# Kernel optimization log

Hardware: AMD Instinct MI355X
Metric: run time of the kernel (lower is better)

Reference implementation:

```python
import jax, jax.numpy as jnp
import numpy as np
from jax import lax

RADIUS = 2  # scipy grey_opening(x, 2): flat 2x2 structuring element


def _grey_opening2d(x, r=RADIUS):
    """Channel-wise grey opening (erosion then dilation) with a flat r x r
    structuring element, matching scipy.ndimage.grey_opening(x, r) with its
    default 'reflect' boundary (edge replication suffices for pad width <= 1
    here; offsets follow scipy's origin convention for even sizes, which makes
    erosion/dilation an adjoint pair so opening(x) <= x and is idempotent).
    x: [B, C, H, W]
    """
    lo = r // 2          # pad-before for erosion (offsets -(r//2) .. r-r//2-1)
    hi = r - 1 - r // 2  # pad-after for erosion
    # erosion: windowed min
    xp = jnp.pad(x, ((0, 0), (0, 0), (lo, hi), (lo, hi)), mode='edge')
    er = lax.reduce_window(xp, jnp.array(jnp.inf, x.dtype), lax.min,
                           (1, 1, r, r), (1, 1, 1, 1), 'VALID')
    # dilation: windowed max with adjoint (mirrored) offsets
    ep = jnp.pad(er, ((0, 0), (0, 0), (hi, lo), (hi, lo)), mode='edge')
    op = lax.reduce_window(ep, jnp.array(-jnp.inf, x.dtype), lax.max,
                           (1, 1, r, r), (1, 1, 1, 1), 'VALID')
    return op


def setup_inputs() -> dict:
    key = jax.random.key(0)
    labels = jax.random.uniform(key, (16, 8, 512, 512), dtype=jnp.float32)
    return {"labels": labels}


def reference(labels):
    smooth = _grey_opening2d(labels)           # detached target in original
    diff = labels - lax.stop_gradient(smooth)
    return jnp.mean(diff * diff)               # nn.MSELoss default 'mean'
```

## Files before the change

### kernel.cpp

```cpp
#include <hip/hip_runtime.h>

#define HH 512
#define WW 512
#define STRIP 16
#define SPI (HH / STRIP)
#define NTASK (128 * SPI)
#define BLOCK 256
#define WPB 4
#define NBLK (NTASK / WPB)
#define NSLOT (STRIP + 2)
#define DEPTH 2
#define NTOTAL (16.0 * 8.0 * 512.0 * 512.0)

__global__ __launch_bounds__(BLOCK, 4) void opening_partial(
    const float* __restrict__ x, float* __restrict__ partial)
{
    const int wb    = (blockIdx.x & 7) * (NBLK / 8) + (blockIdx.x >> 3);
    const int lane  = threadIdx.x & 63;
    const int wid   = wb * WPB + (threadIdx.x >> 6);
    const int img   = wid >> 5;
    const int strip = wid & (SPI - 1);
    const int r0    = strip * STRIP;
    const bool bot  = (strip == SPI - 1);

    const float* ib = x + (size_t)img * (HH * WW);
    const int cA  = lane * 4;
    const int cB  = 256 + lane * 4;
    const int cAm = (lane == 0) ? 0 : cA - 1;
    const int cBm = cB - 1;
    const int cAp = cA + 4;
    const int cBp = (cB + 4 > WW - 1) ? (WW - 1) : (cB + 4);
    const bool rcl = (cB + 4 > WW - 1);

    float RA[NSLOT][6], RB[NSLOT][6];

#define LOADS(s, r)                                                       \
    do {                                                                  \
        const float* rowp = ib + (size_t)(r) * WW;                        \
        const float4 a4 = *(const float4*)(rowp + cA);                    \
        const float4 b4 = *(const float4*)(rowp + cB);                    \
        RA[s][0] = rowp[cAm]; RA[s][1] = a4.x; RA[s][2] = a4.y;           \
        RA[s][3] = a4.z;      RA[s][4] = a4.w; RA[s][5] = rowp[cAp];      \
        RB[s][0] = rowp[cBm]; RB[s][1] = b4.x; RB[s][2] = b4.y;           \
        RB[s][3] = b4.z;      RB[s][4] = b4.w; RB[s][5] = rowp[cBp];      \
    } while (0)

#define RCROW(s, rc)                                                      \
    do {                                                                  \
        rc[0] = fminf(RA[s][0], RA[s][1]); rc[1] = fminf(RA[s][1], RA[s][2]); \
        rc[2] = fminf(RA[s][2], RA[s][3]); rc[3] = fminf(RA[s][3], RA[s][4]); \
        rc[4] = fminf(RA[s][4], RA[s][5]);                                \
        rc[5] = fminf(RB[s][0], RB[s][1]); rc[6] = fminf(RB[s][1], RB[s][2]); \
        rc[7] = fminf(RB[s][2], RB[s][3]); rc[8] = fminf(RB[s][3], RB[s][4]); \
        rc[9] = rcl ? rc[8] : fminf(RB[s][4], RB[s][5]);                  \
    } while (0)

#define CLAMPR(r) (((r) < 0) ? 0 : (((r) > HH - 1) ? (HH - 1) : (r)))

    float rp[10], dp[8];
    float acc = 0.f;

#pragma unroll
    for (int s = 0; s < DEPTH; ++s) LOADS(s, CLAMPR(r0 - 1 + s));

#pragma unroll
    for (int s = 0; s < NSLOT - 1; ++s) {
        if (s + DEPTH < NSLOT) LOADS(s + DEPTH, CLAMPR(r0 - 1 + s + DEPTH));
        float rc[10];
        RCROW(s, rc);
        if (s == 0) {
#pragma unroll
            for (int j = 0; j < 10; ++j) rp[j] = rc[j];
        } else {
            float er[10], d[8];
#pragma unroll
            for (int j = 0; j < 10; ++j) er[j] = fminf(rp[j], rc[j]);
#pragma unroll
            for (int j = 0; j < 4; ++j) {
                d[j]     = fmaxf(er[j], er[j + 1]);
                d[4 + j] = fmaxf(er[5 + j], er[6 + j]);
            }
            if (s >= 2) {
#pragma unroll
                for (int j = 0; j < 4; ++j) {
                    const float oA = fmaxf(dp[j], d[j]);
                    const float oB = fmaxf(dp[4 + j], d[4 + j]);
                    const float fA = RA[s - 1][j + 1] - oA;
                    const float fB = RB[s - 1][j + 1] - oB;
                    acc = fmaf(fA, fA, acc);
                    acc = fmaf(fB, fB, acc);
                }
            }
#pragma unroll
            for (int j = 0; j < 10; ++j) rp[j] = rc[j];
#pragma unroll
            for (int j = 0; j < 8; ++j) dp[j] = d[j];
        }
    }

    if (!bot) {
        float rc[10];
        RCROW(NSLOT - 1, rc);
        float er[10];
#pragma unroll
        for (int j = 0; j < 10; ++j) er[j] = fminf(rp[j], rc[j]);
#pragma unroll
        for (int j = 0; j < 4; ++j) {
            const float dA = fmaxf(er[j], er[j + 1]);
            const float dB = fmaxf(er[5 + j], er[6 + j]);
            const float fA = RA[NSLOT - 2][j + 1] - fmaxf(dp[j], dA);
            const float fB = RB[NSLOT - 2][j + 1] - fmaxf(dp[4 + j], dB);
            acc = fmaf(fA, fA, acc);
            acc = fmaf(fB, fB, acc);
        }
    } else {
#pragma unroll
        for (int j = 0; j < 4; ++j) {
            const float fA = RA[NSLOT - 2][j + 1] - dp[j];
            const float fB = RB[NSLOT - 2][j + 1] - dp[4 + j];
            acc = fmaf(fA, fA, acc);
            acc = fmaf(fB, fB, acc);
        }
    }
#undef LOADS
#undef RCROW
#undef CLAMPR

    __shared__ float wsum[WPB];
#pragma unroll
    for (int off = 32; off; off >>= 1) acc += __shfl_down(acc, off);
    if (lane == 0) wsum[threadIdx.x >> 6] = acc;
    __syncthreads();
    if (threadIdx.x == 0)
        partial[blockIdx.x] = (wsum[0] + wsum[1]) + (wsum[2] + wsum[3]);
}

__global__ __launch_bounds__(256) void reduce_final(
    const float* __restrict__ partial, float* __restrict__ out)
{
    __shared__ double sm[256];
    const int t = threadIdx.x;
    double s = 0.0;
#pragma unroll
    for (int i = 0; i < NBLK / 256; ++i) s += (double)partial[t + 256 * i];
    sm[t] = s;
    __syncthreads();
    for (int h = 128; h > 0; h >>= 1) {
        if (t < h) sm[t] += sm[t + h];
        __syncthreads();
    }
    if (t == 0) out[0] = (float)(sm[0] / NTOTAL);
}

extern "C" void kernel_launch(void* const* d_in, const int* in_sizes, int n_in,
                              void* d_out, int out_size, void* d_ws, size_t ws_size,
                              hipStream_t stream)
{
    const float* x = (const float*)d_in[0];
    float* partial = (float*)d_ws;
    float* out = (float*)d_out;

    opening_partial<<<NBLK, BLOCK, 0, stream>>>(x, partial);
    reduce_final<<<1, 256, 0, stream>>>(partial, out);
}
```

Baseline: 29.06 us.

## Split each strip across two wavefronts, one per image half-width

Each wavefront now covers one 256-column half of a 16-row strip instead of the full 512 columns. This doubles the number of waves and blocks and halves the per-thread register arrays, and the launch bound is raised to 8 blocks per CU to allow higher occupancy. The cost is more redundant halo loads at column and row boundaries, and twice as many partial sums for the final reduction to read.

```diff
diff --git a/kernel.cpp b/kernel.cpp
--- a/kernel.cpp
+++ b/kernel.cpp
@@ -4,7 +4,7 @@
 #define WW 512
 #define STRIP 16
 #define SPI (HH / STRIP)
-#define NTASK (128 * SPI)
+#define NTASK (128 * SPI * 2)
 #define BLOCK 256
 #define WPB 4
 #define NBLK (NTASK / WPB)
@@ -12,52 +12,44 @@
 #define DEPTH 2
 #define NTOTAL (16.0 * 8.0 * 512.0 * 512.0)
 
-__global__ __launch_bounds__(BLOCK, 4) void opening_partial(
+__global__ __launch_bounds__(BLOCK, 8) void opening_partial(
     const float* __restrict__ x, float* __restrict__ partial)
 {
     const int wb    = (blockIdx.x & 7) * (NBLK / 8) + (blockIdx.x >> 3);
     const int lane  = threadIdx.x & 63;
     const int wid   = wb * WPB + (threadIdx.x >> 6);
-    const int img   = wid >> 5;
-    const int strip = wid & (SPI - 1);
+    const int img   = wid >> 6;
+    const int half  = wid & 1;
+    const int strip = (wid >> 1) & (SPI - 1);
     const int r0    = strip * STRIP;
     const bool bot  = (strip == SPI - 1);
 
     const float* ib = x + (size_t)img * (HH * WW);
-    const int cA  = lane * 4;
-    const int cB  = 256 + lane * 4;
-    const int cAm = (lane == 0) ? 0 : cA - 1;
-    const int cBm = cB - 1;
-    const int cAp = cA + 4;
-    const int cBp = (cB + 4 > WW - 1) ? (WW - 1) : (cB + 4);
-    const bool rcl = (cB + 4 > WW - 1);
+    const int c   = half * 256 + lane * 4;
+    const int cm  = (c == 0) ? 0 : c - 1;
+    const int cp  = (c + 4 > WW - 1) ? (WW - 1) : (c + 4);
+    const bool rcl = (c + 4 > WW - 1);
 
-    float RA[NSLOT][6], RB[NSLOT][6];
+    float R[NSLOT][6];
 
 #define LOADS(s, r)                                                       \
     do {                                                                  \
         const float* rowp = ib + (size_t)(r) * WW;                        \
-        const float4 a4 = *(const float4*)(rowp + cA);                    \
-        const float4 b4 = *(const float4*)(rowp + cB);                    \
-        RA[s][0] = rowp[cAm]; RA[s][1] = a4.x; RA[s][2] = a4.y;           \
-        RA[s][3] = a4.z;      RA[s][4] = a4.w; RA[s][5] = rowp[cAp];      \
-        RB[s][0] = rowp[cBm]; RB[s][1] = b4.x; RB[s][2] = b4.y;           \
-        RB[s][3] = b4.z;      RB[s][4] = b4.w; RB[s][5] = rowp[cBp];      \
+        const float4 a4 = *(const float4*)(rowp + c);                     \
+        R[s][0] = rowp[cm]; R[s][1] = a4.x; R[s][2] = a4.y;               \
+        R[s][3] = a4.z;     R[s][4] = a4.w; R[s][5] = rowp[cp];           \
     } while (0)
 
 #define RCROW(s, rc)                                                      \
     do {                                                                  \
-        rc[0] = fminf(RA[s][0], RA[s][1]); rc[1] = fminf(RA[s][1], RA[s][2]); \
-        rc[2] = fminf(RA[s][2], RA[s][3]); rc[3] = fminf(RA[s][3], RA[s][4]); \
-        rc[4] = fminf(RA[s][4], RA[s][5]);                                \
-        rc[5] = fminf(RB[s][0], RB[s][1]); rc[6] = fminf(RB[s][1], RB[s][2]); \
-        rc[7] = fminf(RB[s][2], RB[s][3]); rc[8] = fminf(RB[s][3], RB[s][4]); \
-        rc[9] = rcl ? rc[8] : fminf(RB[s][4], RB[s][5]);                  \
+        rc[0] = fminf(R[s][0], R[s][1]); rc[1] = fminf(R[s][1], R[s][2]); \
+        rc[2] = fminf(R[s][2], R[s][3]); rc[3] = fminf(R[s][3], R[s][4]); \
+        rc[4] = rcl ? rc[3] : fminf(R[s][4], R[s][5]);                    \
     } while (0)
 
 #define CLAMPR(r) (((r) < 0) ? 0 : (((r) > HH - 1) ? (HH - 1) : (r)))
 
-    float rp[10], dp[8];
+    float rp[5], dp[4];
     float acc = 0.f;
 
 #pragma unroll
@@ -66,60 +58,48 @@
 #pragma unroll
     for (int s = 0; s < NSLOT - 1; ++s) {
         if (s + DEPTH < NSLOT) LOADS(s + DEPTH, CLAMPR(r0 - 1 + s + DEPTH));
-        float rc[10];
+        float rc[5];
         RCROW(s, rc);
         if (s == 0) {
 #pragma unroll
-            for (int j = 0; j < 10; ++j) rp[j] = rc[j];
+            for (int j = 0; j < 5; ++j) rp[j] = rc[j];
         } else {
-            float er[10], d[8];
+            float er[5], d[4];
 #pragma unroll
-            for (int j = 0; j < 10; ++j) er[j] = fminf(rp[j], rc[j]);
+            for (int j = 0; j < 5; ++j) er[j] = fminf(rp[j], rc[j]);
 #pragma unroll
-            for (int j = 0; j < 4; ++j) {
-                d[j]     = fmaxf(er[j], er[j + 1]);
-                d[4 + j] = fmaxf(er[5 + j], er[6 + j]);
-            }
+            for (int j = 0; j < 4; ++j) d[j] = fmaxf(er[j], er[j + 1]);
             if (s >= 2) {
 #pragma unroll
                 for (int j = 0; j < 4; ++j) {
-                    const float oA = fmaxf(dp[j], d[j]);
-                    const float oB = fmaxf(dp[4 + j], d[4 + j]);
-                    const float fA = RA[s - 1][j + 1] - oA;
-                    const float fB = RB[s - 1][j + 1] - oB;
-                    acc = fmaf(fA, fA, acc);
-                    acc = fmaf(fB, fB, acc);
+                    const float op = fmaxf(dp[j], d[j]);
+                    const float df = R[s - 1][j + 1] - op;
+                    acc = fmaf(df, df, acc);
                 }
             }
 #pragma unroll
-            for (int j = 0; j < 10; ++j) rp[j] = rc[j];
+            for (int j = 0; j < 5; ++j) rp[j] = rc[j];
 #pragma unroll
-            for (int j = 0; j < 8; ++j) dp[j] = d[j];
+            for (int j = 0; j < 4; ++j) dp[j] = d[j];
         }
     }
 
     if (!bot) {
-        float rc[10];
+        float rc[5], er[5];
         RCROW(NSLOT - 1, rc);
-        float er[10];
 #pragma unroll
-        for (int j = 0; j < 10; ++j) er[j] = fminf(rp[j], rc[j]);
+        for (int j = 0; j < 5; ++j) er[j] = fminf(rp[j], rc[j]);
 #pragma unroll
         for (int j = 0; j < 4; ++j) {
-            const float dA = fmaxf(er[j], er[j + 1]);
-            const float dB = fmaxf(er[5 + j], er[6 + j]);
-            const float fA = RA[NSLOT - 2][j + 1] - fmaxf(dp[j], dA);
-            const float fB = RB[NSLOT - 2][j + 1] - fmaxf(dp[4 + j], dB);
-            acc = fmaf(fA, fA, acc);
-            acc = fmaf(fB, fB, acc);
+            const float d  = fmaxf(er[j], er[j + 1]);
+            const float df = R[NSLOT - 2][j + 1] - fmaxf(dp[j], d);
+            acc = fmaf(df, df, acc);
         }
     } else {
 #pragma unroll
         for (int j = 0; j < 4; ++j) {
-            const float fA = RA[NSLOT - 2][j + 1] - dp[j];
-            const float fB = RB[NSLOT - 2][j + 1] - dp[4 + j];
-            acc = fmaf(fA, fA, acc);
-            acc = fmaf(fB, fB, acc);
+            const float df = R[NSLOT - 2][j + 1] - dp[j];
+            acc = fmaf(df, df, acc);
         }
     }
 #undef LOADS
```

Result: slower. 31.49 us (+8.4%).
